# Performance work log

Measured on AMD Instinct MI355X. Metric: run time of the kernel, lower is better.

The kernel has to match this reference:

```python
import jax, jax.numpy as jnp
import numpy as np

N_EMBD = 768
T_LEN = 4096
BATCH = 4
ATTN_SPAN = 256
LN_EPS = 1e-5
SCALE = float(np.sqrt(N_EMBD * ATTN_SPAN))


def _mlp(x, w1, b1, w2, b2):
    # Linear -> exact GELU -> Linear (weights stored [in, out])
    h = jax.nn.gelu(x @ w1 + b1, approximate=False)
    return h @ w2 + b2


def setup_inputs() -> dict:
    key = jax.random.key(0)
    ks = jax.random.split(key, 16)
    s = 1.0 / np.sqrt(N_EMBD)
    def lin(k):
        kw, kb = jax.random.split(k)
        w = jax.random.uniform(kw, (N_EMBD, N_EMBD), jnp.float32, -s, s)
        b = jax.random.uniform(kb, (N_EMBD,), jnp.float32, -s, s)
        return w, b
    qw1, qb1 = lin(ks[0]); qw2, qb2 = lin(ks[1])
    kw1, kb1 = lin(ks[2]); kw2, kb2 = lin(ks[3])
    vw1, vb1 = lin(ks[4]); vw2, vb2 = lin(ks[5])
    x = jax.random.normal(ks[6], (BATCH, T_LEN, N_EMBD), jnp.float32)
    return {
        'x': x,
        'qw1': qw1, 'qb1': qb1, 'qw2': qw2, 'qb2': qb2,
        'kw1': kw1, 'kb1': kb1, 'kw2': kw2, 'kb2': kb2,
        'vw1': vw1, 'vb1': vb1, 'vw2': vw2, 'vb2': vb2,
        'ln_w': jnp.ones((N_EMBD,), jnp.float32),
        'ln_b': jnp.zeros((N_EMBD,), jnp.float32),
    }


def reference(x, qw1, qb1, qw2, qb2, kw1, kb1, kw2, kb2,
              vw1, vb1, vw2, vb2, ln_w, ln_b):
    T = x.shape[1]
    q = _mlp(x, qw1, qb1, qw2, qb2)
    k = _mlp(x, kw1, kb1, kw2, kb2)
    v = _mlp(x, vw1, vb1, vw2, vb2)
    # full T x T scores then banded causal mask (no softmax), as in source
    scores = jnp.einsum('bid,bjd->bij', q, k) / SCALE
    idx = jnp.arange(T)
    diff = idx[:, None] - idx[None, :]  # i - j
    mask = ((diff >= 0) & (diff < ATTN_SPAN)).astype(scores.dtype)
    scores = scores * mask
    y = jnp.einsum('bij,bjd->bid', scores, v)
    mu = jnp.mean(y, axis=-1, keepdims=True)
    var = jnp.var(y, axis=-1, keepdims=True)
    return (y - mu) * jax.lax.rsqrt(var + LN_EPS) * ln_w + ln_b
```

## Files before the change

### kernel.cpp

```cpp
#include <hip/hip_runtime.h>

typedef _Float16 f16;
typedef _Float16 half8 __attribute__((ext_vector_type(8)));
typedef float float4v __attribute__((ext_vector_type(4)));

#define NE 768
#define N3 2304
#define TT 4096
#define NB 4
#define MM (NB*TT)
#define SPAN 256
#define JW 320

#define GLDS(g, l) __builtin_amdgcn_global_load_lds( \
    (const __attribute__((address_space(1))) void*)(g), \
    (__attribute__((address_space(3))) void*)(l), 16, 0, 0)

__device__ __forceinline__ float gelu_exact(float v){
  return 0.5f * v * (1.0f + erff(v * 0.70710678118654752440f));
}

__global__ __launch_bounds__(256) void cvt_f16_k(const float* __restrict__ in,
                                                 f16* __restrict__ out, int n){
  int i = (blockIdx.x*256 + threadIdx.x)*4;
  if (i >= n) return;
  float4 v = *(const float4*)(in + i);
  struct alignas(8) H4 { f16 a,b,c,d; };
  H4 o; o.a=(f16)v.x; o.b=(f16)v.y; o.c=(f16)v.z; o.d=(f16)v.w;
  *(H4*)(out + i) = o;
}

__global__ __launch_bounds__(256) void transpose_w_k(const float* __restrict__ W,
                                                     f16* __restrict__ Wt){
  __shared__ float tile[32][33];
  int tx = threadIdx.x & 31, ty = threadIdx.x >> 5;
  int bx = blockIdx.x * 32, by = blockIdx.y * 32;
  #pragma unroll
  for (int r=0;r<32;r+=8) tile[ty+r][tx] = W[(size_t)(by+ty+r)*NE + bx + tx];
  __syncthreads();
  #pragma unroll
  for (int r=0;r<32;r+=8) Wt[(size_t)(bx+ty+r)*NE + by + tx] = (f16)tile[tx][ty+r];
}

__global__ void pack3_k(const float* __restrict__ a, const float* __restrict__ b,
                        const float* __restrict__ c, float* __restrict__ o){
  int i = blockIdx.x*256 + threadIdx.x;
  if (i < NE) o[i] = a[i];
  else if (i < 2*NE) o[i] = b[i-NE];
  else if (i < N3) o[i] = c[i-2*NE];
}

__device__ __forceinline__ void gemm_core(
    const f16* __restrict__ A, int lda,
    const f16* __restrict__ Bt,
    int brow, int bcol, f16* As, f16* Bs, float4v (&acc)[4][4])
{
  const int tid  = threadIdx.x;
  const int lane = tid & 63, wave = tid >> 6;
  const int l15 = lane & 15, lk = lane >> 4;
  const int wr = (wave >> 1)*64, wc = (wave & 1)*64;
  const int srow0 = wave*32 + (lane >> 2);
  const int sslot = lane & 3;
  const int fsw = (lk ^ ((l15 >> 1) & 3)) * 8;

  for (int k0 = 0; k0 < NE; k0 += 32){
    #pragma unroll
    for (int t=0; t<2; ++t){
      int r  = srow0 + t*16;
      int sw = (sslot ^ ((r >> 1) & 3)) * 8;
      GLDS(A  + (size_t)(brow + r)*lda + k0 + sw, As + (wave*32 + t*16)*32);
      GLDS(Bt + (size_t)(bcol + r)*NE  + k0 + sw, Bs + (wave*32 + t*16)*32);
    }
    __syncthreads();
    half8 af[4], bf[4];
    #pragma unroll
    for (int i=0;i<4;++i) af[i] = *(const half8*)&As[(wr + i*16 + l15)*32 + fsw];
    #pragma unroll
    for (int j=0;j<4;++j) bf[j] = *(const half8*)&Bs[(wc + j*16 + l15)*32 + fsw];
    #pragma unroll
    for (int i=0;i<4;++i)
      #pragma unroll
      for (int j=0;j<4;++j)
        acc[i][j] = __builtin_amdgcn_mfma_f32_16x16x32_f16(af[i], bf[j], acc[i][j], 0, 0, 0);
    __syncthreads();
  }
}

__global__ __launch_bounds__(256) void gemm_l1_k(
    const f16* __restrict__ A, const f16* __restrict__ Bt,
    const float* __restrict__ bias, f16* __restrict__ Out)
{
  __shared__ f16 smem[8192];
  float4v acc[4][4]{};
  const int brow = blockIdx.x*128, bcol = blockIdx.y*128;
  gemm_core(A, NE, Bt, brow, bcol, smem, smem + 4096, acc);

  const int lane = threadIdx.x & 63, wave = threadIdx.x >> 6;
  const int l15 = lane & 15, lk = lane >> 4;
  const int wr = (wave >> 1)*64, wc = (wave & 1)*64;
  #pragma unroll
  for (int j=0;j<4;++j){
    int col = bcol + wc + j*16 + l15;
    float bv = bias[col];
    #pragma unroll
    for (int i=0;i<4;++i){
      #pragma unroll
      for (int r=0;r<4;++r){
        int row = brow + wr + i*16 + lk*4 + r;
        Out[(size_t)row*N3 + col] = (f16)gelu_exact(acc[i][j][r] + bv);
      }
    }
  }
}

__global__ __launch_bounds__(256) void gemm_l2_k(
    const f16* __restrict__ H, const f16* __restrict__ wt2_all,
    const float* __restrict__ b2_all,
    f16* __restrict__ qh, f16* __restrict__ kh, f16* __restrict__ vt)
{
  __shared__ f16 smem[17408];
  float4v acc[4][4]{};
  const int z = blockIdx.z;
  const int brow = blockIdx.x*128, bcol = blockIdx.y*128;
  gemm_core(H + z*NE, N3, wt2_all + (size_t)z*NE*NE, brow, bcol, smem, smem + 4096, acc);

  const float* bias = b2_all + z*NE;
  const int tid = threadIdx.x, lane = tid & 63, wave = tid >> 6;
  const int l15 = lane & 15, lk = lane >> 4;
  const int wr = (wave >> 1)*64, wc = (wave & 1)*64;

  if (z < 2){
    f16* Out = z ? kh : qh;
    #pragma unroll
    for (int j=0;j<4;++j){
      int col = bcol + wc + j*16 + l15;
      float bv = bias[col];
      #pragma unroll
      for (int i=0;i<4;++i){
        #pragma unroll
        for (int r=0;r<4;++r){
          int row = brow + wr + i*16 + lk*4 + r;
          Out[(size_t)row*NE + col] = (f16)(acc[i][j][r] + bv);
        }
      }
    }
  } else {
    __syncthreads();
    #pragma unroll
    for (int j=0;j<4;++j){
      int cl = wc + j*16 + l15;
      float bv = bias[bcol + cl];
      #pragma unroll
      for (int i=0;i<4;++i){
        #pragma unroll
        for (int r=0;r<4;++r){
          int rl = wr + i*16 + lk*4 + r;
          smem[cl*136 + rl] = (f16)(acc[i][j][r] + bv);
        }
      }
    }
    __syncthreads();
    int b = brow / TT, t0 = brow % TT;
    #pragma unroll
    for (int it=0; it<8; ++it){
      int idx = tid + it*256;
      int c = idx >> 4, rr = (idx & 15)*8;
      half8 v = *(const half8*)&smem[c*136 + rr];
      *(half8*)(vt + (size_t)b*NE*TT + (size_t)(bcol + c)*TT + t0 + rr) = v;
    }
  }
}

__global__ __launch_bounds__(256) void attn_qk_k(
    const f16* __restrict__ Q, const f16* __restrict__ K, f16* __restrict__ S)
{
  __shared__ f16 Ks[JW*40];
  const int tid = threadIdx.x, lane = tid & 63, wave = tid >> 6;
  const int l15 = lane & 15, lk = lane >> 4;
  const int qt = blockIdx.x, b = blockIdx.y;
  const int rowbase = b*TT + qt*64;
  const int jbase = qt*64 - SPAN;
  const int qrow = rowbase + wave*16;

  float4v acc[20]{};

  for (int k0 = 0; k0 < NE; k0 += 32){
    #pragma unroll
    for (int it=0; it<5; ++it){
      int idx = tid + it*256;
      int r = idx >> 2, c = (idx & 3)*8;
      int j = jbase + r;
      half8 v{};
      if (j >= 0) v = *(const half8*)(K + (size_t)(b*TT + j)*NE + k0 + c);
      *(half8*)&Ks[r*40 + c] = v;
    }
    __syncthreads();
    half8 aq = *(const half8*)(Q + (size_t)(qrow + l15)*NE + k0 + lk*8);
    #pragma unroll
    for (int f=0; f<20; ++f){
      half8 bk = *(const half8*)&Ks[(f*16 + l15)*40 + lk*8];
      acc[f] = __builtin_amdgcn_mfma_f32_16x16x32_f16(aq, bk, acc[f], 0, 0, 0);
    }
    __syncthreads();
  }
  const float inv = 1.0f / 443.40500673763256f;
  #pragma unroll
  for (int f=0; f<20; ++f){
    int c = f*16 + l15;
    int jg = jbase + c;
    #pragma unroll
    for (int r=0;r<4;++r){
      int iloc = wave*16 + lk*4 + r;
      int d = (qt*64 + iloc) - jg;
      float v = (d >= 0 && d < SPAN) ? acc[f][r]*inv : 0.0f;
      S[(size_t)(rowbase + iloc)*JW + c] = (f16)v;
    }
  }
}

__global__ __launch_bounds__(256) void attn_pv_k(
    const f16* __restrict__ S, const f16* __restrict__ Vt, float* __restrict__ Y)
{
  __shared__ f16 Vs[64*328];
  const int tid = threadIdx.x, lane = tid & 63, wave = tid >> 6;
  const int l15 = lane & 15, lk = lane >> 4;
  const int qt = blockIdx.x, dc = blockIdx.y, b = blockIdx.z;
  const int d0 = dc*64;
  const int jbase = qt*64 - SPAN;
  const int rowbase = b*TT + qt*64;

  #pragma unroll
  for (int it=0; it<10; ++it){
    int idx = tid + it*256;
    int dd = idx / 40;
    int c = (idx - dd*40)*8;
    int j = jbase + c;
    half8 v{};
    if (j >= 0) v = *(const half8*)(Vt + ((size_t)b*NE + d0 + dd)*TT + j);
    *(half8*)&Vs[dd*328 + c] = v;
  }
  __syncthreads();

  float4v acc[4]{};
  const f16* srow = S + (size_t)(rowbase + wave*16 + l15)*JW;
  #pragma unroll
  for (int kt = 0; kt < JW; kt += 32){
    half8 as = *(const half8*)(srow + kt + lk*8);
    #pragma unroll
    for (int nf=0; nf<4; ++nf){
      half8 bv = *(const half8*)&Vs[(nf*16 + l15)*328 + kt + lk*8];
      acc[nf] = __builtin_amdgcn_mfma_f32_16x16x32_f16(as, bv, acc[nf], 0, 0, 0);
    }
  }
  #pragma unroll
  for (int nf=0; nf<4; ++nf){
    #pragma unroll
    for (int r=0;r<4;++r){
      int row = rowbase + wave*16 + lk*4 + r;
      Y[(size_t)row*NE + d0 + nf*16 + l15] = acc[nf][r];
    }
  }
}

__global__ __launch_bounds__(256) void layernorm_k(
    const float* __restrict__ Y, const float* __restrict__ g,
    const float* __restrict__ be, float* __restrict__ Out)
{
  int row  = blockIdx.x*4 + (threadIdx.x >> 6);
  int lane = threadIdx.x & 63;
  const float* y = Y + (size_t)row*NE;
  float v[12], s=0.f, s2=0.f;
  #pragma unroll
  for (int i=0;i<12;++i){ v[i] = y[lane + i*64]; s += v[i]; s2 += v[i]*v[i]; }
  #pragma unroll
  for (int m=32;m>=1;m>>=1){ s += __shfl_xor(s,m,64); s2 += __shfl_xor(s2,m,64); }
  float mu  = s*(1.f/NE);
  float var = s2*(1.f/NE) - mu*mu;
  float rs  = rsqrtf(var + 1e-5f);
  float* o = Out + (size_t)row*NE;
  #pragma unroll
  for (int i=0;i<12;++i){ int c = lane + i*64; o[c] = (v[i]-mu)*rs*g[c] + be[c]; }
}

extern "C" void kernel_launch(void* const* d_in, const int* in_sizes, int n_in,
                              void* d_out, int out_size, void* d_ws, size_t ws_size,
                              hipStream_t stream)
{
  (void)in_sizes; (void)n_in; (void)out_size; (void)ws_size;
  const float* x     = (const float*)d_in[0];
  const float* w1[3] = {(const float*)d_in[1], (const float*)d_in[5], (const float*)d_in[9]};
  const float* b1[3] = {(const float*)d_in[2], (const float*)d_in[6], (const float*)d_in[10]};
  const float* w2[3] = {(const float*)d_in[3], (const float*)d_in[7], (const float*)d_in[11]};
  const float* b2[3] = {(const float*)d_in[4], (const float*)d_in[8], (const float*)d_in[12]};
  const float* lnw = (const float*)d_in[13];
  const float* lnb = (const float*)d_in[14];

  char* ws = (char*)d_ws;
  size_t off = 0;
  auto alloc = [&](size_t bytes)->void* {
    void* p = ws + off; off += (bytes + 255) & ~size_t(255); return p;
  };
  f16* xh  = (f16*)alloc((size_t)MM*NE*2);
  f16* Ha  = (f16*)alloc((size_t)MM*N3*2);
  f16* qh  = (f16*)alloc((size_t)MM*NE*2);
  f16* kh  = (f16*)alloc((size_t)MM*NE*2);
  f16* vt  = (f16*)alloc((size_t)MM*NE*2);
  f16* wt1 = (f16*)alloc((size_t)N3*NE*2);
  f16* wt2 = (f16*)alloc((size_t)N3*NE*2);
  float* b1a = (float*)alloc((size_t)N3*4);
  float* b2a = (float*)alloc((size_t)N3*4);
  f16*   sb  = xh;
  float* y   = (float*)Ha;

  cvt_f16_k<<<(MM*NE/4 + 255)/256, 256, 0, stream>>>(x, xh, MM*NE);
  dim3 tg(NE/32, NE/32);
  for (int i=0;i<3;++i){
    transpose_w_k<<<tg, 256, 0, stream>>>(w1[i], wt1 + (size_t)i*NE*NE);
    transpose_w_k<<<tg, 256, 0, stream>>>(w2[i], wt2 + (size_t)i*NE*NE);
  }
  pack3_k<<<9, 256, 0, stream>>>(b1[0], b1[1], b1[2], b1a);
  pack3_k<<<9, 256, 0, stream>>>(b2[0], b2[1], b2[2], b2a);

  gemm_l1_k<<<dim3(MM/128, N3/128), 256, 0, stream>>>(xh, wt1, b1a, Ha);
  gemm_l2_k<<<dim3(MM/128, NE/128, 3), 256, 0, stream>>>(Ha, wt2, b2a, qh, kh, vt);

  attn_qk_k<<<dim3(TT/64, NB), 256, 0, stream>>>(qh, kh, sb);
  attn_pv_k<<<dim3(TT/64, NE/64, NB), 256, 0, stream>>>(sb, vt, y);
  layernorm_k<<<MM/4, 256, 0, stream>>>(y, lnw, lnb, (float*)d_out);
}
```

Baseline: 447.0 us.

## Replace MLP GEMMs with 256x256 double-buffered 8-wave pipelined kernels

Both MLP GEMM stages move from 128x128 tiles with 4 waves and single-buffered K=32 steps to 256x256 tiles with 8 waves, K=64 steps and double-buffered LDS (128KB dynamic) loaded via global_load_lds. Loads of the next K tile are interleaved with MFMA quarters using explicit waitcnt, barriers and setprio, and blocks are remapped for L2 locality. Epilogues now stage results through swizzled LDS for coalesced 16-byte stores. The aim is higher MFMA utilization and less global traffic per FLOP. In exchange, the 256-row tiles leave fewer blocks for the available CUs and LDS use is heavy.

```diff
diff --git a/kernel.cpp b/kernel.cpp
--- a/kernel.cpp
+++ b/kernel.cpp
@@ -15,6 +15,11 @@
 #define GLDS(g, l) __builtin_amdgcn_global_load_lds( \
     (const __attribute__((address_space(1))) void*)(g), \
     (__attribute__((address_space(3))) void*)(l), 16, 0, 0)
+
+#define VMW(n) asm volatile("s_waitcnt vmcnt(" #n ")" ::: "memory")
+#define LGKM0() asm volatile("s_waitcnt lgkmcnt(0)" ::: "memory")
+#define SBAR() __builtin_amdgcn_s_barrier()
+#define SCHED0() __builtin_amdgcn_sched_barrier(0)
 
 __device__ __forceinline__ float gelu_exact(float v){
   return 0.5f * v * (1.0f + erff(v * 0.70710678118654752440f));
@@ -50,123 +55,206 @@
   else if (i < N3) o[i] = c[i-2*NE];
 }
 
-__device__ __forceinline__ void gemm_core(
-    const f16* __restrict__ A, int lda,
-    const f16* __restrict__ Bt,
-    int brow, int bcol, f16* As, f16* Bs, float4v (&acc)[4][4])
-{
-  const int tid  = threadIdx.x;
-  const int lane = tid & 63, wave = tid >> 6;
-  const int l15 = lane & 15, lk = lane >> 4;
-  const int wr = (wave >> 1)*64, wc = (wave & 1)*64;
-  const int srow0 = wave*32 + (lane >> 2);
-  const int sslot = lane & 3;
-  const int fsw = (lk ^ ((l15 >> 1) & 3)) * 8;
-
-  for (int k0 = 0; k0 < NE; k0 += 32){
-    #pragma unroll
-    for (int t=0; t<2; ++t){
-      int r  = srow0 + t*16;
-      int sw = (sslot ^ ((r >> 1) & 3)) * 8;
-      GLDS(A  + (size_t)(brow + r)*lda + k0 + sw, As + (wave*32 + t*16)*32);
-      GLDS(Bt + (size_t)(bcol + r)*NE  + k0 + sw, Bs + (wave*32 + t*16)*32);
-    }
-    __syncthreads();
-    half8 af[4], bf[4];
-    #pragma unroll
-    for (int i=0;i<4;++i) af[i] = *(const half8*)&As[(wr + i*16 + l15)*32 + fsw];
-    #pragma unroll
-    for (int j=0;j<4;++j) bf[j] = *(const half8*)&Bs[(wc + j*16 + l15)*32 + fsw];
+
+__device__ __forceinline__ void read_a(half8 (&a)[4][2], const f16* h, int wm, int l15, int lk, int ax){
+  #pragma unroll
+  for (int i=0;i<4;++i){
+    const f16* p = h + (i*32 + wm*16 + l15)*64;
+    a[i][0] = *(const half8*)(p + ((lk*8)     ^ ax));
+    a[i][1] = *(const half8*)(p + ((32+lk*8)  ^ ax));
+  }
+}
+__device__ __forceinline__ void read_b(half8 (&b)[2][2], const f16* h, int wn, int l15, int lk, int ax){
+  #pragma unroll
+  for (int j=0;j<2;++j){
+    const f16* p = h + (j*64 + wn*16 + l15)*64;
+    b[j][0] = *(const half8*)(p + ((lk*8)     ^ ax));
+    b[j][1] = *(const half8*)(p + ((32+lk*8)  ^ ax));
+  }
+}
+
+template<int IB, int JB>
+__device__ __forceinline__ void mfmaq(float4v (&acc)[8][4], half8 (&a)[4][2], half8 (&b)[2][2]){
+  __builtin_amdgcn_s_setprio(1);
+  #pragma unroll
+  for (int kk=0;kk<2;++kk)
     #pragma unroll
     for (int i=0;i<4;++i)
       #pragma unroll
-      for (int j=0;j<4;++j)
-        acc[i][j] = __builtin_amdgcn_mfma_f32_16x16x32_f16(af[i], bf[j], acc[i][j], 0, 0, 0);
-    __syncthreads();
-  }
-}
-
-__global__ __launch_bounds__(256) void gemm_l1_k(
+      for (int j=0;j<2;++j)
+        acc[IB+i][JB+j] = __builtin_amdgcn_mfma_f32_16x16x32_f16(a[i][kk], b[j][kk], acc[IB+i][JB+j], 0, 0, 0);
+  __builtin_amdgcn_s_setprio(0);
+}
+
+#define STG(srcbase, ld, k, dst) do{ \
+  GLDS((srcbase) + (k),                    (dst) + wave*1024); \
+  GLDS((srcbase) + (size_t)8*(ld) + (k),   (dst) + wave*1024 + 512); }while(0)
+
+__device__ __forceinline__ void gemm256_core(
+    const f16* __restrict__ A, int lda, const f16* __restrict__ Bt, int ldb,
+    int brow, int bcol, f16* sh, float4v (&acc)[8][4])
+{
+  const int tid = threadIdx.x, lane = tid&63, wave = tid>>6;
+  const int wm = wave>>2, wn = wave&3, l15 = lane&15, lk = lane>>4;
+  const int ax = (l15&7)*8;
+  half8 a[4][2], b0[2][2], b1[2][2];
+
+  const int rr = wave*16 + (lane>>3);
+  const int ss8 = ((lane&7) ^ (lane>>3))*8;
+  const f16* As0 = A  + (size_t)(brow + rr)*lda + ss8;
+  const f16* As1 = As0 + (size_t)128*lda;
+  const f16* Bs0 = Bt + (size_t)(bcol + rr)*ldb + ss8;
+  const f16* Bs1 = Bs0 + (size_t)128*ldb;
+
+  const int T = NE/64;
+
+  STG(As0, lda, 0, sh + 0);
+  STG(Bs0, ldb, 0, sh + 16384);
+  STG(Bs1, ldb, 0, sh + 16384 + 8192);
+  STG(As1, lda, 0, sh + 8192);
+  VMW(4); SBAR(); SCHED0();
+
+  for (int t=0; t<T-1; ++t){
+    const int cur = t&1, nxt = cur^1;
+    f16* Ac0 = sh + cur*32768;         f16* Ac1 = Ac0 + 8192;
+    f16* Bc0 = Ac0 + 16384;            f16* Bc1 = Bc0 + 8192;
+    f16* An0 = sh + nxt*32768;         f16* An1 = An0 + 8192;
+    f16* Bn0 = An0 + 16384;            f16* Bn1 = Bn0 + 8192;
+    const int k1 = (t+1)*64;
+    read_a(a, Ac0, wm, l15, lk, ax);
+    read_b(b0, Bc0, wn, l15, lk, ax);
+    STG(As0, lda, k1, An0);
+    mfmaq<0,0>(acc, a, b0);
+    VMW(4); SBAR(); SCHED0();
+    read_b(b1, Bc1, wn, l15, lk, ax);
+    STG(Bs0, ldb, k1, Bn0);
+    mfmaq<0,2>(acc, a, b1);
+    VMW(4); SBAR(); SCHED0();
+    read_a(a, Ac1, wm, l15, lk, ax);
+    STG(Bs1, ldb, k1, Bn1);
+    mfmaq<4,2>(acc, a, b1);
+    SBAR(); SCHED0();
+    STG(As1, lda, k1, An1);
+    mfmaq<4,0>(acc, a, b0);
+    VMW(4); SBAR(); SCHED0();
+  }
+  {
+    const int cur = (T-1)&1;
+    f16* Ac0 = sh + cur*32768;         f16* Ac1 = Ac0 + 8192;
+    f16* Bc0 = Ac0 + 16384;            f16* Bc1 = Bc0 + 8192;
+    read_a(a, Ac0, wm, l15, lk, ax);
+    read_b(b0, Bc0, wn, l15, lk, ax);
+    mfmaq<0,0>(acc, a, b0);
+    VMW(2); SBAR(); SCHED0();
+    read_b(b1, Bc1, wn, l15, lk, ax);
+    mfmaq<0,2>(acc, a, b1);
+    VMW(0); SBAR(); SCHED0();
+    read_a(a, Ac1, wm, l15, lk, ax);
+    mfmaq<4,2>(acc, a, b1);
+    LGKM0(); SBAR(); SCHED0();
+    mfmaq<4,0>(acc, a, b0);
+  }
+}
+
+__global__ __launch_bounds__(512, 2) void gemm8_l1_k(
     const f16* __restrict__ A, const f16* __restrict__ Bt,
     const float* __restrict__ bias, f16* __restrict__ Out)
 {
-  __shared__ f16 smem[8192];
-  float4v acc[4][4]{};
-  const int brow = blockIdx.x*128, bcol = blockIdx.y*128;
-  gemm_core(A, NE, Bt, brow, bcol, smem, smem + 4096, acc);
-
-  const int lane = threadIdx.x & 63, wave = threadIdx.x >> 6;
-  const int l15 = lane & 15, lk = lane >> 4;
-  const int wr = (wave >> 1)*64, wc = (wave & 1)*64;
+  extern __shared__ __align__(16) f16 sh[];
+  const int tid = threadIdx.x, lane = tid&63, wave = tid>>6;
+  const int wm = wave>>2, wn = wave&3, l15 = lane&15, lk = lane>>4;
+  int bid = blockIdx.y*64 + blockIdx.x;
+  int L = (bid&7)*72 + (bid>>3);
+  int brow = (L/9)*256, bcol = (L%9)*256;
+
+  float4v acc[8][4]{};
+  gemm256_core(A, NE, Bt, NE, brow, bcol, sh, acc);
+
   #pragma unroll
   for (int j=0;j<4;++j){
-    int col = bcol + wc + j*16 + l15;
-    float bv = bias[col];
-    #pragma unroll
-    for (int i=0;i<4;++i){
+    int col = j*64 + wn*16 + l15;
+    float bv = bias[bcol+col];
+    #pragma unroll
+    for (int i=0;i<8;++i){
       #pragma unroll
       for (int r=0;r<4;++r){
-        int row = brow + wr + i*16 + lk*4 + r;
-        Out[(size_t)row*N3 + col] = (f16)gelu_exact(acc[i][j][r] + bv);
+        int row = i*32 + wm*16 + lk*4 + r;
+        sh[row*256 + (col ^ ((row&7)<<3))] = (f16)gelu_exact(acc[i][j][r] + bv);
       }
     }
   }
-}
-
-__global__ __launch_bounds__(256) void gemm_l2_k(
+  SBAR();
+  #pragma unroll
+  for (int it=0;it<16;++it){
+    int idx = tid + it*512;
+    int row = idx>>5, cc = (idx&31)*8;
+    half8 v = *(const half8*)(sh + row*256 + (cc ^ ((row&7)<<3)));
+    *(half8*)(Out + (size_t)(brow+row)*N3 + bcol + cc) = v;
+  }
+}
+
+__global__ __launch_bounds__(512, 2) void gemm8_l2_k(
     const f16* __restrict__ H, const f16* __restrict__ wt2_all,
     const float* __restrict__ b2_all,
     f16* __restrict__ qh, f16* __restrict__ kh, f16* __restrict__ vt)
 {
-  __shared__ f16 smem[17408];
-  float4v acc[4][4]{};
+  extern __shared__ __align__(16) f16 sh[];
+  const int tid = threadIdx.x, lane = tid&63, wave = tid>>6;
+  const int wm = wave>>2, wn = wave&3, l15 = lane&15, lk = lane>>4;
   const int z = blockIdx.z;
-  const int brow = blockIdx.x*128, bcol = blockIdx.y*128;
-  gemm_core(H + z*NE, N3, wt2_all + (size_t)z*NE*NE, brow, bcol, smem, smem + 4096, acc);
+  int bid = blockIdx.y*64 + blockIdx.x;
+  int L = (bid&7)*24 + (bid>>3);
+  int brow = (L/3)*256, bcol = (L%3)*256;
+
+  float4v acc[8][4]{};
+  gemm256_core(H + z*NE, N3, wt2_all + (size_t)z*NE*NE, NE, brow, bcol, sh, acc);
 
   const float* bias = b2_all + z*NE;
-  const int tid = threadIdx.x, lane = tid & 63, wave = tid >> 6;
-  const int l15 = lane & 15, lk = lane >> 4;
-  const int wr = (wave >> 1)*64, wc = (wave & 1)*64;
-
   if (z < 2){
     f16* Out = z ? kh : qh;
     #pragma unroll
     for (int j=0;j<4;++j){
-      int col = bcol + wc + j*16 + l15;
-      float bv = bias[col];
+      int col = j*64 + wn*16 + l15;
+      float bv = bias[bcol+col];
       #pragma unroll
-      for (int i=0;i<4;++i){
+      for (int i=0;i<8;++i){
         #pragma unroll
         for (int r=0;r<4;++r){
-          int row = brow + wr + i*16 + lk*4 + r;
-          Out[(size_t)row*NE + col] = (f16)(acc[i][j][r] + bv);
+          int row = i*32 + wm*16 + lk*4 + r;
+          sh[row*256 + (col ^ ((row&7)<<3))] = (f16)(acc[i][j][r] + bv);
         }
       }
     }
+    SBAR();
+    #pragma unroll
+    for (int it=0;it<16;++it){
+      int idx = tid + it*512;
+      int row = idx>>5, cc = (idx&31)*8;
+      half8 v = *(const half8*)(sh + row*256 + (cc ^ ((row&7)<<3)));
+      *(half8*)(Out + (size_t)(brow+row)*NE + bcol + cc) = v;
+    }
   } else {
-    __syncthreads();
     #pragma unroll
     for (int j=0;j<4;++j){
-      int cl = wc + j*16 + l15;
-      float bv = bias[bcol + cl];
+      int col = j*64 + wn*16 + l15;
+      float bv = bias[bcol+col];
       #pragma unroll
-      for (int i=0;i<4;++i){
+      for (int i=0;i<8;++i){
         #pragma unroll
         for (int r=0;r<4;++r){
-          int rl = wr + i*16 + lk*4 + r;
-          smem[cl*136 + rl] = (f16)(acc[i][j][r] + bv);
+          int row = i*32 + wm*16 + lk*4 + r;
+          sh[col*256 + (row ^ ((col&7)<<3))] = (f16)(acc[i][j][r] + bv);
         }
       }
     }
-    __syncthreads();
+    SBAR();
     int b = brow / TT, t0 = brow % TT;
     #pragma unroll
-    for (int it=0; it<8; ++it){
-      int idx = tid + it*256;
-      int c = idx >> 4, rr = (idx & 15)*8;
-      half8 v = *(const half8*)&smem[c*136 + rr];
-      *(half8*)(vt + (size_t)b*NE*TT + (size_t)(bcol + c)*TT + t0 + rr) = v;
+    for (int it=0;it<16;++it){
+      int idx = tid + it*512;
+      int col = idx>>5, rc = (idx&31)*8;
+      half8 v = *(const half8*)(sh + col*256 + (rc ^ ((col&7)<<3)));
+      *(half8*)(vt + (size_t)b*NE*TT + (size_t)(bcol+col)*TT + t0 + rc) = v;
     }
   }
 }
@@ -312,6 +400,13 @@
   f16*   sb  = xh;
   float* y   = (float*)Ha;
 
+  static bool attr_done = false;
+  hipFuncSetAttribute(reinterpret_cast<const void*>(&gemm8_l1_k),
+                      hipFuncAttributeMaxDynamicSharedMemorySize, 131072);
+  hipFuncSetAttribute(reinterpret_cast<const void*>(&gemm8_l2_k),
+                      hipFuncAttributeMaxDynamicSharedMemorySize, 131072);
+  (void)attr_done;
+
   cvt_f16_k<<<(MM*NE/4 + 255)/256, 256, 0, stream>>>(x, xh, MM*NE);
   dim3 tg(NE/32, NE/32);
   for (int i=0;i<3;++i){
@@ -321,8 +416,8 @@
   pack3_k<<<9, 256, 0, stream>>>(b1[0], b1[1], b1[2], b1a);
   pack3_k<<<9, 256, 0, stream>>>(b2[0], b2[1], b2[2], b2a);
 
-  gemm_l1_k<<<dim3(MM/128, N3/128), 256, 0, stream>>>(xh, wt1, b1a, Ha);
-  gemm_l2_k<<<dim3(MM/128, NE/128, 3), 256, 0, stream>>>(Ha, wt2, b2a, qh, kh, vt);
+  gemm8_l1_k<<<dim3(64, 9), 512, 131072, stream>>>(xh, wt1, b1a, Ha);
+  gemm8_l2_k<<<dim3(64, 3, 3), 512, 131072, stream>>>(Ha, wt2, b2a, qh, kh, vt);
 
   attn_qk_k<<<dim3(TT/64, NB), 256, 0, stream>>>(qh, kh, sb);
   attn_pv_k<<<dim3(TT/64, NE/64, NB), 256, 0, stream>>>(sb, vt, y);
```

Result: faster. 433.3 us (-3.1%).

## Stage GEMM epilogues through swizzled LDS, remap blocks across XCDs, merge prep kernels

Applied to the files above, without the earlier changes.

The GEMM epilogues now write results into XOR-swizzled shared memory and then issue coalesced 16-byte global stores, replacing scattered 2-byte stores. The V-transpose path uses packed 4-element LDS writes. Block indices are remapped with an (bid&7) stride so neighbouring tiles share an XCD's L2 cache. The six weight transposes and two bias packs are merged into single launches to cut launch overhead. In exchange, each block does an extra LDS round trip and barrier, and gemm_l1 uses more shared memory.

```diff
diff --git a/kernel.cpp b/kernel.cpp
--- a/kernel.cpp
+++ b/kernel.cpp
@@ -20,19 +20,26 @@
   return 0.5f * v * (1.0f + erff(v * 0.70710678118654752440f));
 }
 
+struct alignas(8) H4 { f16 a,b,c,d; };
+
 __global__ __launch_bounds__(256) void cvt_f16_k(const float* __restrict__ in,
                                                  f16* __restrict__ out, int n){
   int i = (blockIdx.x*256 + threadIdx.x)*4;
   if (i >= n) return;
   float4 v = *(const float4*)(in + i);
-  struct alignas(8) H4 { f16 a,b,c,d; };
   H4 o; o.a=(f16)v.x; o.b=(f16)v.y; o.c=(f16)v.z; o.d=(f16)v.w;
   *(H4*)(out + i) = o;
 }
 
-__global__ __launch_bounds__(256) void transpose_w_k(const float* __restrict__ W,
-                                                     f16* __restrict__ Wt){
+__global__ __launch_bounds__(256) void transpose_w6_k(
+    const float* __restrict__ w0, const float* __restrict__ w1,
+    const float* __restrict__ w2, const float* __restrict__ w3,
+    const float* __restrict__ w4, const float* __restrict__ w5,
+    f16* __restrict__ wt1, f16* __restrict__ wt2){
   __shared__ float tile[32][33];
+  int z = blockIdx.z;
+  const float* W = z==0?w0 : z==1?w1 : z==2?w2 : z==3?w3 : z==4?w4 : w5;
+  f16* Wt = (z<3 ? wt1 + (size_t)z*NE*NE : wt2 + (size_t)(z-3)*NE*NE);
   int tx = threadIdx.x & 31, ty = threadIdx.x >> 5;
   int bx = blockIdx.x * 32, by = blockIdx.y * 32;
   #pragma unroll
@@ -42,12 +49,19 @@
   for (int r=0;r<32;r+=8) Wt[(size_t)(bx+ty+r)*NE + by + tx] = (f16)tile[tx][ty+r];
 }
 
-__global__ void pack3_k(const float* __restrict__ a, const float* __restrict__ b,
-                        const float* __restrict__ c, float* __restrict__ o){
+__global__ void packb_k(const float* __restrict__ a0, const float* __restrict__ a1,
+                        const float* __restrict__ a2, const float* __restrict__ c0,
+                        const float* __restrict__ c1, const float* __restrict__ c2,
+                        float* __restrict__ o1, float* __restrict__ o2){
   int i = blockIdx.x*256 + threadIdx.x;
-  if (i < NE) o[i] = a[i];
-  else if (i < 2*NE) o[i] = b[i-NE];
-  else if (i < N3) o[i] = c[i-2*NE];
+  if (i < N3){
+    const float* s = (i<NE) ? a0 : (i<2*NE ? a1 : a2);
+    o1[i] = s[i % NE];
+  } else if (i < 2*N3){
+    int k = i - N3;
+    const float* s = (k<NE) ? c0 : (k<2*NE ? c1 : c2);
+    o2[k] = s[k % NE];
+  }
 }
 
 __device__ __forceinline__ void gemm_core(
@@ -90,26 +104,36 @@
     const f16* __restrict__ A, const f16* __restrict__ Bt,
     const float* __restrict__ bias, f16* __restrict__ Out)
 {
-  __shared__ f16 smem[8192];
+  __shared__ f16 smem[16384];
   float4v acc[4][4]{};
-  const int brow = blockIdx.x*128, bcol = blockIdx.y*128;
+  const int bid = blockIdx.x;
+  const int L = (bid & 7)*288 + (bid >> 3);
+  const int brow = (L/18)*128, bcol = (L%18)*128;
   gemm_core(A, NE, Bt, brow, bcol, smem, smem + 4096, acc);
 
-  const int lane = threadIdx.x & 63, wave = threadIdx.x >> 6;
+  const int tid = threadIdx.x, lane = tid & 63, wave = tid >> 6;
   const int l15 = lane & 15, lk = lane >> 4;
   const int wr = (wave >> 1)*64, wc = (wave & 1)*64;
   #pragma unroll
   for (int j=0;j<4;++j){
-    int col = bcol + wc + j*16 + l15;
-    float bv = bias[col];
+    int col = wc + j*16 + l15;
+    float bv = bias[bcol + col];
     #pragma unroll
     for (int i=0;i<4;++i){
       #pragma unroll
       for (int r=0;r<4;++r){
-        int row = brow + wr + i*16 + lk*4 + r;
-        Out[(size_t)row*N3 + col] = (f16)gelu_exact(acc[i][j][r] + bv);
+        int row = wr + i*16 + lk*4 + r;
+        smem[row*128 + (col ^ ((row&7)<<3))] = (f16)gelu_exact(acc[i][j][r] + bv);
       }
     }
+  }
+  __syncthreads();
+  #pragma unroll
+  for (int it=0; it<8; ++it){
+    int idx = tid + it*256;
+    int row = idx >> 4, cc = (idx & 15)*8;
+    half8 v = *(const half8*)&smem[row*128 + (cc ^ ((row&7)<<3))];
+    *(half8*)(Out + (size_t)(brow + row)*N3 + bcol + cc) = v;
   }
 }
 
@@ -118,10 +142,12 @@
     const float* __restrict__ b2_all,
     f16* __restrict__ qh, f16* __restrict__ kh, f16* __restrict__ vt)
 {
-  __shared__ f16 smem[17408];
+  __shared__ f16 smem[16384];
   float4v acc[4][4]{};
   const int z = blockIdx.z;
-  const int brow = blockIdx.x*128, bcol = blockIdx.y*128;
+  const int bid = blockIdx.x;
+  const int L = (bid & 7)*96 + (bid >> 3);
+  const int brow = (L/6)*128, bcol = (L%6)*128;
   gemm_core(H + z*NE, N3, wt2_all + (size_t)z*NE*NE, brow, bcol, smem, smem + 4096, acc);
 
   const float* bias = b2_all + z*NE;
@@ -133,30 +159,36 @@
     f16* Out = z ? kh : qh;
     #pragma unroll
     for (int j=0;j<4;++j){
-      int col = bcol + wc + j*16 + l15;
-      float bv = bias[col];
+      int col = wc + j*16 + l15;
+      float bv = bias[bcol + col];
       #pragma unroll
       for (int i=0;i<4;++i){
         #pragma unroll
         for (int r=0;r<4;++r){
-          int row = brow + wr + i*16 + lk*4 + r;
-          Out[(size_t)row*NE + col] = (f16)(acc[i][j][r] + bv);
+          int row = wr + i*16 + lk*4 + r;
+          smem[row*128 + (col ^ ((row&7)<<3))] = (f16)(acc[i][j][r] + bv);
         }
       }
     }
+    __syncthreads();
+    #pragma unroll
+    for (int it=0; it<8; ++it){
+      int idx = tid + it*256;
+      int row = idx >> 4, cc = (idx & 15)*8;
+      half8 v = *(const half8*)&smem[row*128 + (cc ^ ((row&7)<<3))];
+      *(half8*)(Out + (size_t)(brow + row)*NE + bcol + cc) = v;
+    }
   } else {
-    __syncthreads();
     #pragma unroll
     for (int j=0;j<4;++j){
       int cl = wc + j*16 + l15;
       float bv = bias[bcol + cl];
       #pragma unroll
       for (int i=0;i<4;++i){
-        #pragma unroll
-        for (int r=0;r<4;++r){
-          int rl = wr + i*16 + lk*4 + r;
-          smem[cl*136 + rl] = (f16)(acc[i][j][r] + bv);
-        }
+        int r0 = wr + i*16 + lk*4;
+        H4 p; p.a = (f16)(acc[i][j][0] + bv); p.b = (f16)(acc[i][j][1] + bv);
+              p.c = (f16)(acc[i][j][2] + bv); p.d = (f16)(acc[i][j][3] + bv);
+        *(H4*)&smem[cl*128 + (r0 ^ ((cl&7)<<3))] = p;
       }
     }
     __syncthreads();
@@ -164,9 +196,9 @@
     #pragma unroll
     for (int it=0; it<8; ++it){
       int idx = tid + it*256;
-      int c = idx >> 4, rr = (idx & 15)*8;
-      half8 v = *(const half8*)&smem[c*136 + rr];
-      *(half8*)(vt + (size_t)b*NE*TT + (size_t)(bcol + c)*TT + t0 + rr) = v;
+      int col = idx >> 4, rc = (idx & 15)*8;
+      half8 v = *(const half8*)&smem[col*128 + (rc ^ ((col&7)<<3))];
+      *(half8*)(vt + (size_t)b*NE*TT + (size_t)(bcol + col)*TT + t0 + rc) = v;
     }
   }
 }
@@ -313,16 +345,12 @@
   float* y   = (float*)Ha;
 
   cvt_f16_k<<<(MM*NE/4 + 255)/256, 256, 0, stream>>>(x, xh, MM*NE);
-  dim3 tg(NE/32, NE/32);
-  for (int i=0;i<3;++i){
-    transpose_w_k<<<tg, 256, 0, stream>>>(w1[i], wt1 + (size_t)i*NE*NE);
-    transpose_w_k<<<tg, 256, 0, stream>>>(w2[i], wt2 + (size_t)i*NE*NE);
-  }
-  pack3_k<<<9, 256, 0, stream>>>(b1[0], b1[1], b1[2], b1a);
-  pack3_k<<<9, 256, 0, stream>>>(b2[0], b2[1], b2[2], b2a);
-
-  gemm_l1_k<<<dim3(MM/128, N3/128), 256, 0, stream>>>(xh, wt1, b1a, Ha);
-  gemm_l2_k<<<dim3(MM/128, NE/128, 3), 256, 0, stream>>>(Ha, wt2, b2a, qh, kh, vt);
+  transpose_w6_k<<<dim3(NE/32, NE/32, 6), 256, 0, stream>>>(
+      w1[0], w1[1], w1[2], w2[0], w2[1], w2[2], wt1, wt2);
+  packb_k<<<18, 256, 0, stream>>>(b1[0], b1[1], b1[2], b2[0], b2[1], b2[2], b1a, b2a);
+
+  gemm_l1_k<<<dim3(MM/128 * N3/128), 256, 0, stream>>>(xh, wt1, b1a, Ha);
+  gemm_l2_k<<<dim3(MM/128 * NE/128, 1, 3), 256, 0, stream>>>(Ha, wt2, b2a, qh, kh, vt);
 
   attn_qk_k<<<dim3(TT/64, NB), 256, 0, stream>>>(qh, kh, sb);
   attn_pv_k<<<dim3(TT/64, NE/64, NB), 256, 0, stream>>>(sb, vt, y);
```

After: 427.4 us. 4.4% less time.
